# Performance work log

Measured on AMD Instinct MI355X. Metric: run time of the kernel, lower is better.

The kernel has to match this reference:

```python
import jax, jax.numpy as jnp
import numpy as np

ALPHA = 0.03
RETURN_WEIGHT = 0.6
SHARPE_WEIGHT = 0.4
WINDOW = 20  # min(20, N//4) == 20 for N = 2**21
N = 2097152


def setup_inputs() -> dict:
    key = jax.random.key(0)
    k1, k2 = jax.random.split(key)
    predictions = jax.random.normal(k1, (N, 1), dtype=jnp.float32)
    returns = jax.random.normal(k2, (N,), dtype=jnp.float32) * 0.02  # daily-return scale
    return {"predictions": predictions, "returns": returns}


def _std(x):
    # torch.std uses the unbiased estimator (ddof=1)
    return jnp.std(x, ddof=1)


def _forward(predictions, returns):
    signals = jnp.tanh(predictions)                 # [N, 1]
    r = returns * signals.squeeze(-1)               # [N] portfolio returns
    n = r.shape[0]

    mean_return = jnp.mean(r)
    std_return = _std(r) + 1e-8
    base_sharpe = mean_return / std_return

    # Rolling std over trailing WINDOW (vectorized form of the python loop):
    # window k covers r[k : k+WINDOW], k in [0, n-WINDOW)
    win = jnp.stack([r[j:n - WINDOW + j] for j in range(WINDOW)], axis=-1)  # [n-W, W]
    rolling_vol = jnp.std(win, axis=-1, ddof=1)
    vol_stability = 1.0 / (_std(rolling_vol) + 1e-6)
    enhanced_sharpe = base_sharpe * (1.0 + 0.1 * vol_stability)

    return_magnitude = jnp.mean(jnp.abs(r))
    positive_frequency = jnp.mean((r > 0).astype(r.dtype))

    dr = r[1:] - r[:-1]
    return_smoothness = 1.0 / (jnp.mean(jnp.abs(dr)) + 1e-6)
    momentum_consistency = jnp.mean(jnp.sign(r[1:]) * jnp.sign(r[:-1]))

    cum = jnp.cumsum(r)
    running_max = jax.lax.cummax(cum, axis=0)
    max_drawdown = jnp.max(running_max - cum)
    drawdown_penalty = jax.nn.relu(max_drawdown - 0.05)

    sorted_r = jnp.sort(r)
    cvar_samples = max(1, int(n * ALPHA))
    cvar = -jnp.mean(sorted_r[:cvar_samples])

    ds = signals[1:] - signals[:-1]
    signal_changes = jnp.mean(jnp.abs(ds))
    signal_smoothness = 1.0 / (signal_changes + 1e-6)

    sharpe_components = (0.4 * enhanced_sharpe
                         + 0.25 * return_magnitude
                         + 0.15 * positive_frequency
                         + 0.1 * momentum_consistency
                         + 0.05 * return_smoothness
                         + 0.05 * signal_smoothness)
    risk_penalties = 0.05 * cvar + 0.02 * drawdown_penalty + 0.01 * signal_changes

    return -(RETURN_WEIGHT * return_magnitude
             + SHARPE_WEIGHT * sharpe_components
             - risk_penalties)


def reference(predictions, returns):
    return _forward(predictions, returns)
```

## Files before the change

kernel.cpp:

```cpp
#include <hip/hip_runtime.h>
#include <math.h>

#define N_TOTAL 2097152
#define WINDOW  20
#define M_ROLL  (N_TOTAL - WINDOW)
#define K_CVAR  62914u

#define BS      512
#define TILE    4096
#define NB_MAIN (N_TOTAL / TILE)
#define NBINS   1024
#define NSUB    4
#define LPAD    8
#define NGCOPY  8
#define CB      512

#define HG_OFF   0
#define SEN_OFF  32768
#define DDT_OFF  32832
#define PBS_OFF  49216

__device__ __forceinline__ unsigned ordkey(float f) {
    unsigned b = __float_as_uint(f);
    return (b & 0x80000000u) ? ~b : (b | 0x80000000u);
}
__device__ __forceinline__ float inv_ordkey(unsigned u) {
    return __uint_as_float((u & 0x80000000u) ? (u ^ 0x80000000u) : ~u);
}
__device__ __forceinline__ float sgnf(float x) {
    return (x > 0.f) ? 1.f : ((x < 0.f) ? -1.f : 0.f);
}
__device__ __forceinline__ float fast_tanh(float x) {
    float ax = fabsf(x);
    float e = __expf(2.0f * ax);
    float t = 1.0f - 2.0f * __builtin_amdgcn_rcpf(e + 1.0f);
    return copysignf(t, x);
}
__device__ __forceinline__ double bin_mid(int b) {
    unsigned klo = ((unsigned)b) << 22;
    unsigned khi = (b == NBINS - 1) ? 0xFFFFFFFFu : (((unsigned)(b + 1)) << 22);
    return 0.5 * ((double)inv_ordkey(klo) + (double)inv_ordkey(khi));
}

template<int CTRL>
__device__ __forceinline__ float dpp_f(float x, float old) {
    return __int_as_float(__builtin_amdgcn_update_dpp(
        __float_as_int(old), __float_as_int(x), CTRL, 0xf, 0xf, false));
}
__device__ __forceinline__ float wsum63(float x) {
    x += dpp_f<0x111>(x, 0.f);
    x += dpp_f<0x112>(x, 0.f);
    x += dpp_f<0x114>(x, 0.f);
    x += dpp_f<0x118>(x, 0.f);
    x += dpp_f<0x142>(x, 0.f);
    x += dpp_f<0x143>(x, 0.f);
    return x;
}

#define NINF (-__builtin_huge_valf())
#define PINF ( __builtin_huge_valf())

__global__ __launch_bounds__(BS, 4) void k_main(const float* __restrict__ pred,
                                                const float* __restrict__ ret,
                                                unsigned* __restrict__ hg,
                                                double* __restrict__ ddt,
                                                float* __restrict__ pbs)
{
    __shared__ __align__(16) float sh_r[TILE + 24];
    __shared__ __align__(16) unsigned lh[NSUB][NBINS + LPAD];
    __shared__ float sred[8][9];
    __shared__ float4 stup[8];
    __shared__ float swb[8];

    const int tid = threadIdx.x;
    const int lane = tid & 63, wid = tid >> 6;
    const int tileStart = blockIdx.x * TILE;
    const int t8 = tid * 8;
    const int sub = (tid >> 4) & (NSUB - 1);

    for (int b = tid; b < NSUB * (NBINS + LPAD) / 4; b += BS)
        ((uint4*)lh)[b] = make_uint4(0u, 0u, 0u, 0u);

    float4 pa = *(const float4*)(pred + tileStart + t8);
    float4 pb = *(const float4*)(pred + tileStart + t8 + 4);
    float4 qa = *(const float4*)(ret  + tileStart + t8);
    float4 qb = *(const float4*)(ret  + tileStart + t8 + 4);
    const bool halo = (tid >= 1 && tid < 6);
    float4 hp = make_float4(0.f,0.f,0.f,0.f), hq = hp;
    if (halo) {
        int g = tileStart + TILE + 4 * (tid - 1);
        if (g + 3 < N_TOTAL) { hp = *(const float4*)(pred + g); hq = *(const float4*)(ret + g); }
    }
    float pm1 = 0.f, qm1 = 0.f;
    if (tid == 0 && tileStart > 0) { pm1 = pred[tileStart - 1]; qm1 = ret[tileStart - 1]; }

    float pe[8] = {pa.x, pa.y, pa.z, pa.w, pb.x, pb.y, pb.z, pb.w};
    float qe[8] = {qa.x, qa.y, qa.z, qa.w, qb.x, qb.y, qb.z, qb.w};
    float sg[8], rr[8];
#pragma unroll
    for (int j = 0; j < 8; ++j) { sg[j] = fast_tanh(pe[j]); rr[j] = qe[j] * sg[j]; }
    *(float4*)&sh_r[t8]     = make_float4(rr[0], rr[1], rr[2], rr[3]);
    *(float4*)&sh_r[t8 + 4] = make_float4(rr[4], rr[5], rr[6], rr[7]);
    if (lane == 63) swb[wid] = sg[7];
    if (halo) {
        float h0 = fast_tanh(hp.x), h1 = fast_tanh(hp.y);
        float h2 = fast_tanh(hp.z), h3 = fast_tanh(hp.w);
        *(float4*)&sh_r[TILE + 4 * (tid - 1)] =
            make_float4(hq.x * h0, hq.y * h1, hq.z * h2, hq.w * h3);
    }
    __syncthreads();

    const int iBase = tileStart + t8;

    float sprev = __shfl_up(sg[7], 1);
    float rm1 = 0.f, sm1 = 0.f;
    if (tid == 0) {
        if (tileStart > 0) { sm1 = fast_tanh(pm1); rm1 = qm1 * sm1; }
    } else {
        rm1 = sh_r[t8 - 1];
        sm1 = (lane == 0) ? swb[wid - 1] : sprev;
    }

    float4 w1 = *(float4*)&sh_r[t8 + 8];
    float4 w2 = *(float4*)&sh_r[t8 + 12];
    float4 w3 = *(float4*)&sh_r[t8 + 16];
    float4 w4 = *(float4*)&sh_r[t8 + 20];
    float4 w5 = *(float4*)&sh_r[t8 + 24];

    float sum_r = 0.f, sum_r2 = 0.f, sum_ab = 0.f, cnt_p = 0.f;
#pragma unroll
    for (int j = 0; j < 8; ++j) {
        sum_r  += rr[j];
        sum_r2 += rr[j] * rr[j];
        sum_ab += fabsf(rr[j]);
        cnt_p  += (rr[j] > 0.f) ? 1.f : 0.f;
    }
    float sum_adr = 0.f, sum_sgn = 0.f, sum_ads = 0.f;
#pragma unroll
    for (int j = 1; j < 8; ++j) {
        sum_adr += fabsf(rr[j] - rr[j-1]);
        sum_sgn += sgnf(rr[j]) * sgnf(rr[j-1]);
        sum_ads += fabsf(sg[j] - sg[j-1]);
    }
    if (iBase >= 1) {
        sum_adr += fabsf(rr[0] - rm1);
        sum_sgn += sgnf(rr[0]) * sgnf(rm1);
        sum_ads += fabsf(sg[0] - sm1);
    }

#pragma unroll
    for (int j = 0; j < 8; ++j)
        atomicAdd(&lh[sub][ordkey(rr[j]) >> 22], 1u);

    float vsum = 0.f, vsqr = 0.f;
    {
        float ws = 0.f, wq = 0.f;
#pragma unroll
        for (int j = 0; j < 8; ++j) { ws += rr[j]; wq += rr[j]*rr[j]; }
        ws += w1.x + w1.y + w1.z + w1.w;
        wq += w1.x*w1.x + w1.y*w1.y + w1.z*w1.z + w1.w*w1.w;
        ws += w2.x + w2.y + w2.z + w2.w;
        wq += w2.x*w2.x + w2.y*w2.y + w2.z*w2.z + w2.w*w2.w;
        ws += w3.x + w3.y + w3.z + w3.w;
        wq += w3.x*w3.x + w3.y*w3.y + w3.z*w3.z + w3.w*w3.w;

        float inc[7] = {w4.x, w4.y, w4.z, w4.w, w5.x, w5.y, w5.z};

        if (iBase + 0 < M_ROLL) {
            float var = fmaxf((wq - ws*ws*(1.0f/WINDOW)) * (1.0f/(WINDOW-1)), 0.f);
            vsum += sqrtf(var); vsqr += var;
        }
#pragma unroll
        for (int k = 1; k < 8; ++k) {
            ws += inc[k-1] - rr[k-1];
            wq += inc[k-1]*inc[k-1] - rr[k-1]*rr[k-1];
            if (iBase + k < M_ROLL) {
                float var = fmaxf((wq - ws*ws*(1.0f/WINDOW)) * (1.0f/(WINDOW-1)), 0.f);
                vsum += sqrtf(var); vsqr += var;
            }
        }
    }

    float tS = rr[0], tMP = rr[0], tMN = rr[0], tDD = 0.f;
#pragma unroll
    for (int j = 1; j < 8; ++j) {
        tS += rr[j]; tMP = fmaxf(tMP, tS); tMN = fminf(tMN, tS); tDD = fmaxf(tDD, tMP - tS);
    }
#define DD_STEP(CTRL) do {                                          \
        float iS  = dpp_f<CTRL>(tS,  0.f);                          \
        float iMP = dpp_f<CTRL>(tMP, NINF);                         \
        float iMN = dpp_f<CTRL>(tMN, PINF);                         \
        float iDD = dpp_f<CTRL>(tDD, 0.f);                          \
        float nDD = fmaxf(fmaxf(iDD, tDD), iMP - (iS + tMN));       \
        float nMP = fmaxf(iMP, iS + tMP);                           \
        float nMN = fminf(iMN, iS + tMN);                           \
        tS = iS + tS; tMP = nMP; tMN = nMN; tDD = nDD;              \
    } while (0)
    DD_STEP(0x111);
    DD_STEP(0x112);
    DD_STEP(0x114);
    DD_STEP(0x118);
    DD_STEP(0x142);
    DD_STEP(0x143);
#undef DD_STEP

    sum_r  = wsum63(sum_r);   sum_r2 = wsum63(sum_r2);
    sum_ab = wsum63(sum_ab);  cnt_p  = wsum63(cnt_p);
    sum_adr= wsum63(sum_adr); sum_sgn= wsum63(sum_sgn);
    sum_ads= wsum63(sum_ads); vsum   = wsum63(vsum);
    vsqr   = wsum63(vsqr);

    if (lane == 63) {
        sred[wid][0]=sum_r;  sred[wid][1]=sum_r2; sred[wid][2]=sum_ab;
        sred[wid][3]=cnt_p;  sred[wid][4]=sum_adr; sred[wid][5]=sum_sgn;
        sred[wid][6]=sum_ads; sred[wid][7]=vsum;   sred[wid][8]=vsqr;
        stup[wid] = make_float4(tS, tMP, tMN, tDD);
    }
    __syncthreads();

    if (tid < 9) {
        float tot = 0.f;
        for (int w = 0; w < 8; ++w) tot += sred[w][tid];
        pbs[blockIdx.x * 16 + tid] = tot;
    }
    if (tid == 0) {
        float4 a = stup[0];
        double bS = a.x, bMP = a.y, bMN = a.z, bDD = a.w;
        for (int w = 1; w < 8; ++w) {
            float4 b = stup[w];
            double nDD = fmax(fmax(bDD, (double)b.w), bMP - (bS + (double)b.z));
            double nMP = fmax(bMP, bS + (double)b.y);
            double nMN = fmin(bMN, bS + (double)b.z);
            bS += (double)b.x; bMP = nMP; bMN = nMN; bDD = nDD;
        }
        double2* dd2 = (double2*)ddt;
        dd2[2 * blockIdx.x]     = make_double2(bS, bMP);
        dd2[2 * blockIdx.x + 1] = make_double2(bMN, bDD);
    }
    {
        unsigned* gh = hg + (blockIdx.x & (NGCOPY - 1)) * NBINS;
        for (int b = tid; b < NBINS; b += BS) {
            unsigned v = lh[0][b] + lh[1][b] + lh[2][b] + lh[3][b];
            if (v) atomicAdd(&gh[b], v);
        }
    }
}

__global__ __launch_bounds__(CB) void k_combine(const unsigned* __restrict__ hg,
                                                const unsigned* __restrict__ sen,
                                                const double* __restrict__ ddt,
                                                const float* __restrict__ pbs,
                                                float* __restrict__ out)
{
    __shared__ double s_dd[8][4];
    __shared__ double s_sc[8][9];
    __shared__ double s_ds[8];
    __shared__ unsigned s_wt[8];
    __shared__ int s_edge;
    __shared__ unsigned s_cb, s_ce;

    const int t = threadIdx.x;
    const int lane = t & 63, wid = t >> 6;

    {
        const double2* dd2 = (const double2*)ddt;
        double2 a0 = dd2[2 * t], a1 = dd2[2 * t + 1];
        double S = a0.x, MP = a0.y, MN = a1.x, DD = a1.y;
        for (int off = 1; off < 64; off <<= 1) {
            double oS  = __shfl_down(S,  off);
            double oMP = __shfl_down(MP, off);
            double oMN = __shfl_down(MN, off);
            double oDD = __shfl_down(DD, off);
            double nDD = fmax(fmax(DD, oDD), MP - (S + oMN));
            double nMP = fmax(MP, S + oMP);
            double nMN = fmin(MN, S + oMN);
            S += oS; MP = nMP; MN = nMN; DD = nDD;
        }
        if (lane == 0) { s_dd[wid][0]=S; s_dd[wid][1]=MP; s_dd[wid][2]=MN; s_dd[wid][3]=DD; }
    }
    {
        const float* pb = pbs + t * 16;
        double d0=pb[0],d1=pb[1],d2=pb[2],d3=pb[3],d4=pb[4],d5=pb[5],d6=pb[6],d7=pb[7],d8=pb[8];
        for (int off = 1; off < 64; off <<= 1) {
            d0+=__shfl_down(d0,off); d1+=__shfl_down(d1,off); d2+=__shfl_down(d2,off);
            d3+=__shfl_down(d3,off); d4+=__shfl_down(d4,off); d5+=__shfl_down(d5,off);
            d6+=__shfl_down(d6,off); d7+=__shfl_down(d7,off); d8+=__shfl_down(d8,off);
        }
        if (lane == 0) {
            s_sc[wid][0]=d0; s_sc[wid][1]=d1; s_sc[wid][2]=d2; s_sc[wid][3]=d3;
            s_sc[wid][4]=d4; s_sc[wid][5]=d5; s_sc[wid][6]=d6; s_sc[wid][7]=d7; s_sc[wid][8]=d8;
        }
    }
    unsigned base = sen[0];
    int b0 = 2 * t, b1 = 2 * t + 1;
    unsigned cnt0, cnt1, cntt;
    double sum0 = 0.0, sum1 = 0.0;
    {
        unsigned h0 = 0u, h1 = 0u;
        for (int c = 0; c < NGCOPY; ++c) {
            uint2 hh = *(const uint2*)&hg[c * NBINS + b0];
            h0 += hh.x; h1 += hh.y;
        }
        unsigned subv = base * (unsigned)NGCOPY;
        cnt0 = h0 - subv;
        cnt1 = h1 - subv;
        if (cnt0) sum0 = (double)cnt0 * bin_mid(b0);
        if (cnt1) sum1 = (double)cnt1 * bin_mid(b1);
        cntt = cnt0 + cnt1;
    }
    unsigned v = cntt;
    for (int off = 1; off < 64; off <<= 1) {
        unsigned y = __shfl_up(v, off);
        if (lane >= off) v += y;
    }
    if (lane == 63) s_wt[wid] = v;
    __syncthreads();
    {
        unsigned woff = 0;
        for (int w = 0; w < wid; ++w) woff += s_wt[w];
        unsigned incl = v + woff, excl = incl - cntt;
        if (excl < K_CVAR && excl + cnt0 >= K_CVAR)      { s_edge = b0; s_cb = excl;        s_ce = cnt0; }
        else if (excl + cnt0 < K_CVAR && incl >= K_CVAR) { s_edge = b1; s_cb = excl + cnt0; s_ce = cnt1; }
    }
    __syncthreads();
    const int be = s_edge;
    const unsigned cb = s_cb, ce = s_ce;

    double part = 0.0;
    if (b0 < be) part += sum0;
    if (b1 < be) part += sum1;
    for (int off = 1; off < 64; off <<= 1) part += __shfl_down(part, off);
    if (lane == 0) s_ds[wid] = part;
    __syncthreads();

    if (t == 0) {
        double gS = s_dd[0][0], gMP = s_dd[0][1], gMN = s_dd[0][2], gDD = s_dd[0][3];
        for (int w = 1; w < 8; ++w) {
            double xS = s_dd[w][0], xMP = s_dd[w][1], xMN = s_dd[w][2], xDD = s_dd[w][3];
            double nDD = fmax(fmax(gDD, xDD), gMP - (gS + xMN));
            double nMP = fmax(gMP, gS + xMP);
            double nMN = fmin(gMN, gS + xMN);
            gS += xS; gMP = nMP; gMN = nMN; gDD = nDD;
        }
        double S1=0,S2=0,S3=0,S4=0,S5=0,S6=0,S7=0,V1=0,V2=0;
        for (int w = 0; w < 8; ++w) {
            S1+=s_sc[w][0]; S2+=s_sc[w][1]; S3+=s_sc[w][2]; S4+=s_sc[w][3];
            S5+=s_sc[w][4]; S6+=s_sc[w][5]; S7+=s_sc[w][6]; V1+=s_sc[w][7]; V2+=s_sc[w][8];
        }
        double bsum = 0.0;
        for (int w = 0; w < 8; ++w) bsum += s_ds[w];

        double n = (double)N_TOTAL;
        double mean_r = S1 / n;
        double var_r = (S2 - S1 * S1 / n) / (n - 1.0);
        if (var_r < 0.0) var_r = 0.0;
        double std_r = sqrt(var_r) + 1e-8;
        double base_sharpe = mean_r / std_r;

        double m = (double)M_ROLL;
        double var_v = (V2 - V1 * V1 / m) / (m - 1.0);
        if (var_v < 0.0) var_v = 0.0;
        double vs = 1.0 / (sqrt(var_v) + 1e-6);
        double es = base_sharpe * (1.0 + 0.1 * vs);

        double rm = S3 / n;
        double pf = S4 / n;
        double rs = 1.0 / (S5 / (n - 1.0) + 1e-6);
        double mc = S6 / (n - 1.0);
        double dd = fmax(gDD, 0.0);
        double ddp = dd - 0.05; if (ddp < 0.0) ddp = 0.0;
        double sc = S7 / (n - 1.0);
        double ss = 1.0 / (sc + 1e-6);

        double mneed = (double)(K_CVAR - cb);
        double elo = (double)inv_ordkey(((unsigned)be) << 22);
        double ehi = (double)inv_ordkey(((unsigned)(be + 1)) << 22);
        double edgev = elo + (mneed / (2.0 * (double)(ce > 0u ? ce : 1u))) * (ehi - elo);
        double cvar = -(bsum + mneed * edgev) / (double)K_CVAR;

        double SC = 0.4 * es + 0.25 * rm + 0.15 * pf + 0.1 * mc + 0.05 * rs + 0.05 * ss;
        double RP = 0.05 * cvar + 0.02 * ddp + 0.01 * sc;
        out[0] = (float)(-(0.6 * rm + 0.4 * SC - RP));
    }
}

extern "C" void kernel_launch(void* const* d_in, const int* in_sizes, int n_in,
                              void* d_out, int out_size, void* d_ws, size_t ws_size,
                              hipStream_t stream)
{
    const float* pred = (const float*)d_in[0];
    const float* ret  = (const float*)d_in[1];
    char* ws = (char*)d_ws;
    unsigned* hg  = (unsigned*)(ws + HG_OFF);
    unsigned* sen = (unsigned*)(ws + SEN_OFF);
    double*   ddt = (double*)(ws + DDT_OFF);
    float*    pbs = (float*)(ws + PBS_OFF);

    k_main<<<NB_MAIN, BS, 0, stream>>>(pred, ret, hg, ddt, pbs);
    k_combine<<<1, CB, 0, stream>>>(hg, sen, ddt, pbs, (float*)d_out);
}
```

Measured before the change: 79.29 us.

## Fuse combine kernel into main via last-block atomic ticket; widen LDS histogram copies

Merges the single-block combine kernel into the main kernel. Each block publishes its partials with atomics and increments a ready counter, and the last block to arrive does the final reduction, which removes a second kernel launch and its gap. The LDS histogram is also split into 8 sub-copies with an odd stride to reduce bank and atomic contention. The cost is extra atomic traffic, a vmcnt wait in every block, and reliance on a never-reset counter measured against a sentinel.

```diff
diff --git a/kernel.cpp b/kernel.cpp
--- a/kernel.cpp
+++ b/kernel.cpp
@@ -10,15 +10,15 @@
 #define TILE    4096
 #define NB_MAIN (N_TOTAL / TILE)
 #define NBINS   1024
-#define NSUB    4
-#define LPAD    8
+#define NSUB    8
+#define LSTRIDE (NBINS + 5)
 #define NGCOPY  8
-#define CB      512
 
 #define HG_OFF   0
 #define SEN_OFF  32768
-#define DDT_OFF  32832
-#define PBS_OFF  49216
+#define RDY_OFF  32832
+#define DDT_OFF  32896
+#define PBS_OFF  49280
 
 __device__ __forceinline__ unsigned ordkey(float f) {
     unsigned b = __float_as_uint(f);
@@ -60,25 +60,31 @@
 #define NINF (-__builtin_huge_valf())
 #define PINF ( __builtin_huge_valf())
 
-__global__ __launch_bounds__(BS, 4) void k_main(const float* __restrict__ pred,
-                                                const float* __restrict__ ret,
-                                                unsigned* __restrict__ hg,
-                                                double* __restrict__ ddt,
-                                                float* __restrict__ pbs)
+__global__ __launch_bounds__(BS, 4) void k_all(const float* __restrict__ pred,
+                                               const float* __restrict__ ret,
+                                               unsigned* __restrict__ hg,
+                                               const unsigned* __restrict__ sen,
+                                               unsigned* __restrict__ rdy,
+                                               double* __restrict__ ddt,
+                                               float* __restrict__ pbs,
+                                               float* __restrict__ out)
 {
     __shared__ __align__(16) float sh_r[TILE + 24];
-    __shared__ __align__(16) unsigned lh[NSUB][NBINS + LPAD];
+    __shared__ __align__(16) unsigned lh[NSUB][LSTRIDE];
     __shared__ float sred[8][9];
     __shared__ float4 stup[8];
     __shared__ float swb[8];
+    __shared__ unsigned s_last;
 
     const int tid = threadIdx.x;
     const int lane = tid & 63, wid = tid >> 6;
     const int tileStart = blockIdx.x * TILE;
     const int t8 = tid * 8;
-    const int sub = (tid >> 4) & (NSUB - 1);
-
-    for (int b = tid; b < NSUB * (NBINS + LPAD) / 4; b += BS)
+    const int sub = (tid >> 3) & (NSUB - 1);
+
+    const unsigned senv = sen[0];
+
+    for (int b = tid; b < NSUB * LSTRIDE / 4; b += BS)
         ((uint4*)lh)[b] = make_uint4(0u, 0u, 0u, 0u);
 
     float4 pa = *(const float4*)(pred + tileStart + t8);
@@ -218,10 +224,19 @@
     }
     __syncthreads();
 
+    {
+        unsigned* gh = hg + (blockIdx.x & (NGCOPY - 1)) * NBINS;
+        for (int b = tid; b < NBINS; b += BS) {
+            unsigned v = 0;
+#pragma unroll
+            for (int s = 0; s < NSUB; ++s) v += lh[s][b];
+            if (v) atomicAdd(&gh[b], v);
+        }
+    }
     if (tid < 9) {
         float tot = 0.f;
         for (int w = 0; w < 8; ++w) tot += sred[w][tid];
-        pbs[blockIdx.x * 16 + tid] = tot;
+        atomicExch((unsigned*)&pbs[blockIdx.x * 16 + tid], __float_as_uint(tot));
     }
     if (tid == 0) {
         float4 a = stup[0];
@@ -233,39 +248,50 @@
             double nMN = fmin(bMN, bS + (double)b.z);
             bS += (double)b.x; bMP = nMP; bMN = nMN; bDD = nDD;
         }
-        double2* dd2 = (double2*)ddt;
-        dd2[2 * blockIdx.x]     = make_double2(bS, bMP);
-        dd2[2 * blockIdx.x + 1] = make_double2(bMN, bDD);
-    }
-    {
-        unsigned* gh = hg + (blockIdx.x & (NGCOPY - 1)) * NBINS;
-        for (int b = tid; b < NBINS; b += BS) {
-            unsigned v = lh[0][b] + lh[1][b] + lh[2][b] + lh[3][b];
-            if (v) atomicAdd(&gh[b], v);
-        }
-    }
-}
-
-__global__ __launch_bounds__(CB) void k_combine(const unsigned* __restrict__ hg,
-                                                const unsigned* __restrict__ sen,
-                                                const double* __restrict__ ddt,
-                                                const float* __restrict__ pbs,
-                                                float* __restrict__ out)
-{
-    __shared__ double s_dd[8][4];
-    __shared__ double s_sc[8][9];
-    __shared__ double s_ds[8];
-    __shared__ unsigned s_wt[8];
-    __shared__ int s_edge;
-    __shared__ unsigned s_cb, s_ce;
-
-    const int t = threadIdx.x;
-    const int lane = t & 63, wid = t >> 6;
-
-    {
-        const double2* dd2 = (const double2*)ddt;
-        double2 a0 = dd2[2 * t], a1 = dd2[2 * t + 1];
-        double S = a0.x, MP = a0.y, MN = a1.x, DD = a1.y;
+        unsigned long long* d8 = (unsigned long long*)(ddt + 4 * blockIdx.x);
+        atomicExch(&d8[0], (unsigned long long)__double_as_longlong(bS));
+        atomicExch(&d8[1], (unsigned long long)__double_as_longlong(bMP));
+        atomicExch(&d8[2], (unsigned long long)__double_as_longlong(bMN));
+        atomicExch(&d8[3], (unsigned long long)__double_as_longlong(bDD));
+    }
+
+    asm volatile("s_waitcnt vmcnt(0)" ::: "memory");
+    __syncthreads();
+    if (tid == 0) {
+        unsigned old = atomicAdd(rdy, 1u);
+        s_last = (old - senv == (unsigned)(NB_MAIN - 1)) ? 1u : 0u;
+    }
+    __syncthreads();
+    if (!s_last) return;
+
+    __shared__ double c_dd[8][4];
+    __shared__ double c_sc[8][9];
+    __shared__ double c_ds[8];
+    __shared__ unsigned c_wt[8];
+    __shared__ int c_edge;
+    __shared__ unsigned c_cb, c_ce;
+
+    const int t = tid;
+
+    unsigned long long* dd8 = (unsigned long long*)ddt;
+    unsigned long long A0 = atomicAdd(&dd8[4*t + 0], 0ULL);
+    unsigned long long A1 = atomicAdd(&dd8[4*t + 1], 0ULL);
+    unsigned long long A2 = atomicAdd(&dd8[4*t + 2], 0ULL);
+    unsigned long long A3 = atomicAdd(&dd8[4*t + 3], 0ULL);
+    unsigned* pbu = (unsigned*)pbs;
+    unsigned Bv[9];
+#pragma unroll
+    for (int k = 0; k < 9; ++k) Bv[k] = atomicAdd(&pbu[16*t + k], 0u);
+    unsigned long long* hg8 = (unsigned long long*)hg;
+    unsigned long long Cv[NGCOPY];
+#pragma unroll
+    for (int c = 0; c < NGCOPY; ++c) Cv[c] = atomicAdd(&hg8[c * (NBINS/2) + t], 0ULL);
+
+    {
+        double S = __longlong_as_double((long long)A0);
+        double MP = __longlong_as_double((long long)A1);
+        double MN = __longlong_as_double((long long)A2);
+        double DD = __longlong_as_double((long long)A3);
         for (int off = 1; off < 64; off <<= 1) {
             double oS  = __shfl_down(S,  off);
             double oMP = __shfl_down(MP, off);
@@ -276,32 +302,35 @@
             double nMN = fmin(MN, S + oMN);
             S += oS; MP = nMP; MN = nMN; DD = nDD;
         }
-        if (lane == 0) { s_dd[wid][0]=S; s_dd[wid][1]=MP; s_dd[wid][2]=MN; s_dd[wid][3]=DD; }
-    }
-    {
-        const float* pb = pbs + t * 16;
-        double d0=pb[0],d1=pb[1],d2=pb[2],d3=pb[3],d4=pb[4],d5=pb[5],d6=pb[6],d7=pb[7],d8=pb[8];
+        if (lane == 0) { c_dd[wid][0]=S; c_dd[wid][1]=MP; c_dd[wid][2]=MN; c_dd[wid][3]=DD; }
+    }
+    {
+        double d0=(double)__uint_as_float(Bv[0]), d1=(double)__uint_as_float(Bv[1]);
+        double d2=(double)__uint_as_float(Bv[2]), d3=(double)__uint_as_float(Bv[3]);
+        double d4=(double)__uint_as_float(Bv[4]), d5=(double)__uint_as_float(Bv[5]);
+        double d6=(double)__uint_as_float(Bv[6]), d7=(double)__uint_as_float(Bv[7]);
+        double d8=(double)__uint_as_float(Bv[8]);
         for (int off = 1; off < 64; off <<= 1) {
             d0+=__shfl_down(d0,off); d1+=__shfl_down(d1,off); d2+=__shfl_down(d2,off);
             d3+=__shfl_down(d3,off); d4+=__shfl_down(d4,off); d5+=__shfl_down(d5,off);
             d6+=__shfl_down(d6,off); d7+=__shfl_down(d7,off); d8+=__shfl_down(d8,off);
         }
         if (lane == 0) {
-            s_sc[wid][0]=d0; s_sc[wid][1]=d1; s_sc[wid][2]=d2; s_sc[wid][3]=d3;
-            s_sc[wid][4]=d4; s_sc[wid][5]=d5; s_sc[wid][6]=d6; s_sc[wid][7]=d7; s_sc[wid][8]=d8;
-        }
-    }
-    unsigned base = sen[0];
+            c_sc[wid][0]=d0; c_sc[wid][1]=d1; c_sc[wid][2]=d2; c_sc[wid][3]=d3;
+            c_sc[wid][4]=d4; c_sc[wid][5]=d5; c_sc[wid][6]=d6; c_sc[wid][7]=d7; c_sc[wid][8]=d8;
+        }
+    }
     int b0 = 2 * t, b1 = 2 * t + 1;
     unsigned cnt0, cnt1, cntt;
     double sum0 = 0.0, sum1 = 0.0;
     {
         unsigned h0 = 0u, h1 = 0u;
+#pragma unroll
         for (int c = 0; c < NGCOPY; ++c) {
-            uint2 hh = *(const uint2*)&hg[c * NBINS + b0];
-            h0 += hh.x; h1 += hh.y;
-        }
-        unsigned subv = base * (unsigned)NGCOPY;
+            h0 += (unsigned)(Cv[c] & 0xffffffffull);
+            h1 += (unsigned)(Cv[c] >> 32);
+        }
+        unsigned subv = senv * (unsigned)NGCOPY;
         cnt0 = h0 - subv;
         cnt1 = h1 - subv;
         if (cnt0) sum0 = (double)cnt0 * bin_mid(b0);
@@ -313,30 +342,30 @@
         unsigned y = __shfl_up(v, off);
         if (lane >= off) v += y;
     }
-    if (lane == 63) s_wt[wid] = v;
+    if (lane == 63) c_wt[wid] = v;
     __syncthreads();
     {
         unsigned woff = 0;
-        for (int w = 0; w < wid; ++w) woff += s_wt[w];
+        for (int w = 0; w < wid; ++w) woff += c_wt[w];
         unsigned incl = v + woff, excl = incl - cntt;
-        if (excl < K_CVAR && excl + cnt0 >= K_CVAR)      { s_edge = b0; s_cb = excl;        s_ce = cnt0; }
-        else if (excl + cnt0 < K_CVAR && incl >= K_CVAR) { s_edge = b1; s_cb = excl + cnt0; s_ce = cnt1; }
-    }
-    __syncthreads();
-    const int be = s_edge;
-    const unsigned cb = s_cb, ce = s_ce;
+        if (excl < K_CVAR && excl + cnt0 >= K_CVAR)      { c_edge = b0; c_cb = excl;        c_ce = cnt0; }
+        else if (excl + cnt0 < K_CVAR && incl >= K_CVAR) { c_edge = b1; c_cb = excl + cnt0; c_ce = cnt1; }
+    }
+    __syncthreads();
+    const int be = c_edge;
+    const unsigned cb = c_cb, ce = c_ce;
 
     double part = 0.0;
     if (b0 < be) part += sum0;
     if (b1 < be) part += sum1;
     for (int off = 1; off < 64; off <<= 1) part += __shfl_down(part, off);
-    if (lane == 0) s_ds[wid] = part;
+    if (lane == 0) c_ds[wid] = part;
     __syncthreads();
 
     if (t == 0) {
-        double gS = s_dd[0][0], gMP = s_dd[0][1], gMN = s_dd[0][2], gDD = s_dd[0][3];
+        double gS = c_dd[0][0], gMP = c_dd[0][1], gMN = c_dd[0][2], gDD = c_dd[0][3];
         for (int w = 1; w < 8; ++w) {
-            double xS = s_dd[w][0], xMP = s_dd[w][1], xMN = s_dd[w][2], xDD = s_dd[w][3];
+            double xS = c_dd[w][0], xMP = c_dd[w][1], xMN = c_dd[w][2], xDD = c_dd[w][3];
             double nDD = fmax(fmax(gDD, xDD), gMP - (gS + xMN));
             double nMP = fmax(gMP, gS + xMP);
             double nMN = fmin(gMN, gS + xMN);
@@ -344,11 +373,11 @@
         }
         double S1=0,S2=0,S3=0,S4=0,S5=0,S6=0,S7=0,V1=0,V2=0;
         for (int w = 0; w < 8; ++w) {
-            S1+=s_sc[w][0]; S2+=s_sc[w][1]; S3+=s_sc[w][2]; S4+=s_sc[w][3];
-            S5+=s_sc[w][4]; S6+=s_sc[w][5]; S7+=s_sc[w][6]; V1+=s_sc[w][7]; V2+=s_sc[w][8];
+            S1+=c_sc[w][0]; S2+=c_sc[w][1]; S3+=c_sc[w][2]; S4+=c_sc[w][3];
+            S5+=c_sc[w][4]; S6+=c_sc[w][5]; S7+=c_sc[w][6]; V1+=c_sc[w][7]; V2+=c_sc[w][8];
         }
         double bsum = 0.0;
-        for (int w = 0; w < 8; ++w) bsum += s_ds[w];
+        for (int w = 0; w < 8; ++w) bsum += c_ds[w];
 
         double n = (double)N_TOTAL;
         double mean_r = S1 / n;
@@ -393,9 +422,9 @@
     char* ws = (char*)d_ws;
     unsigned* hg  = (unsigned*)(ws + HG_OFF);
     unsigned* sen = (unsigned*)(ws + SEN_OFF);
+    unsigned* rdy = (unsigned*)(ws + RDY_OFF);
     double*   ddt = (double*)(ws + DDT_OFF);
     float*    pbs = (float*)(ws + PBS_OFF);
 
-    k_main<<<NB_MAIN, BS, 0, stream>>>(pred, ret, hg, ddt, pbs);
-    k_combine<<<1, CB, 0, stream>>>(hg, sen, ddt, pbs, (float*)d_out);
-}
+    k_all<<<NB_MAIN, BS, 0, stream>>>(pred, ret, hg, sen, rdy, ddt, pbs, (float*)d_out);
+}
```

New measurement: 81.62 us. +2.9%, slower.
